# Optimization experiments

Hardware: AMD Instinct MI355X
Metric: run time of the kernel (lower is better)

The kernel has to match this reference:

```python
import jax, jax.numpy as jnp
import numpy as np

EMBED_DIM = 1024
NUM_HEADS = 16
HEAD_DIM = EMBED_DIM // NUM_HEADS
B, T = 4, 2048


def setup_inputs() -> dict:
    key = jax.random.key(0)
    k1, k2, k3, k4, k5 = jax.random.split(key, 5)
    s = 0.02
    return {
        "x": jax.random.normal(k1, (B, T, EMBED_DIM), dtype=jnp.float32),
        "w_qkv": jax.random.normal(k2, (EMBED_DIM, 3 * EMBED_DIM), dtype=jnp.float32) * s,
        "b_qkv": jnp.zeros((3 * EMBED_DIM,), dtype=jnp.float32),
        "w_proj": jax.random.normal(k3, (EMBED_DIM, EMBED_DIM), dtype=jnp.float32) * s,
        "b_proj": jnp.zeros((EMBED_DIM,), dtype=jnp.float32),
    }


def reference(x, w_qkv, b_qkv, w_proj, b_proj):
    Bx, Tx, C = x.shape
    H, D = NUM_HEADS, HEAD_DIM
    qkv = x @ w_qkv + b_qkv                      # [B,T,3C]
    qkv = qkv.reshape(Bx, Tx, 3, H, D)
    q = qkv[:, :, 0].transpose(0, 2, 1, 3)       # [B,H,T,D]
    k = qkv[:, :, 1].transpose(0, 2, 1, 3)
    v = qkv[:, :, 2].transpose(0, 2, 1, 3)
    scale = 1.0 / jnp.sqrt(jnp.asarray(D, dtype=x.dtype))
    att = jnp.einsum("bhqd,bhkd->bhqk", q, k) * scale   # [B,H,T,T]
    causal = jnp.tril(jnp.ones((Tx, Tx), dtype=bool))
    att = jnp.where(causal[None, None], att, jnp.asarray(-jnp.inf, dtype=att.dtype))
    att = jax.nn.softmax(att, axis=-1)
    y = jnp.einsum("bhqk,bhkd->bhqd", att, v)            # [B,H,T,D]
    y = y.transpose(0, 2, 1, 3).reshape(Bx, Tx, C)
    return y @ w_proj + b_proj
```

## Files before the change

### kernel.cpp

```cpp
#include <hip/hip_runtime.h>
#include <hip/hip_bf16.h>

typedef __bf16 bf16_t;
typedef __attribute__((ext_vector_type(4))) __bf16 bf16x4;
typedef __attribute__((ext_vector_type(8))) __bf16 bf16x8;
typedef __attribute__((ext_vector_type(4))) float f32x4;
typedef __attribute__((ext_vector_type(16))) float f32x16;
typedef __attribute__((ext_vector_type(4))) unsigned int uint4v;

__device__ __forceinline__ void async_copy16(const void* g, void* lds) {
  __builtin_amdgcn_global_load_lds(
      (const __attribute__((address_space(1))) unsigned int*)g,
      (__attribute__((address_space(3))) unsigned int*)lds, 16, 0, 0);
}

__device__ __forceinline__ unsigned pkbf(float lo, float hi) {
  unsigned short a = __builtin_bit_cast(unsigned short, (bf16_t)lo);
  unsigned short b = __builtin_bit_cast(unsigned short, (bf16_t)hi);
  return (unsigned)a | ((unsigned)b << 16);
}

__device__ __forceinline__ float swap_add(float v) {
  return v + __shfl_xor(v, 32);
}

__global__ __launch_bounds__(256) void cast_f32_bf16(
    const float* __restrict__ in, bf16_t* __restrict__ out, long n8) {
  long i = (long)blockIdx.x * blockDim.x + threadIdx.x;
  if (i >= n8) return;
  const float4* p = (const float4*)(in + i * 8);
  float4 a = p[0], b = p[1];
  bf16x8 o;
  o[0] = (bf16_t)a.x; o[1] = (bf16_t)a.y; o[2] = (bf16_t)a.z; o[3] = (bf16_t)a.w;
  o[4] = (bf16_t)b.x; o[5] = (bf16_t)b.y; o[6] = (bf16_t)b.z; o[7] = (bf16_t)b.w;
  *(bf16x8*)(out + i * 8) = o;
}

__global__ __launch_bounds__(256) void transpose_cast(
    const float* __restrict__ in, bf16_t* __restrict__ out, int R, int C) {
  __shared__ float tile[32][33];
  int r0 = blockIdx.y * 32, c0 = blockIdx.x * 32;
  int tx = threadIdx.x, ty = threadIdx.y;
#pragma unroll
  for (int j = 0; j < 32; j += 8)
    tile[ty + j][tx] = in[(size_t)(r0 + ty + j) * C + c0 + tx];
  __syncthreads();
#pragma unroll
  for (int j = 0; j < 32; j += 8)
    out[(size_t)(c0 + ty + j) * R + r0 + tx] = (bf16_t)tile[tx][ty + j];
}

template <int MODE>
__global__ __launch_bounds__(256, 2) void gemm_db(
    const bf16_t* __restrict__ A, const bf16_t* __restrict__ Bt,
    const float* __restrict__ bias, int M, int N, int K,
    bf16_t* __restrict__ Qo, bf16_t* __restrict__ Ko, bf16_t* __restrict__ Vo,
    float* __restrict__ Fo) {
  constexpr int BK = 64;
  __shared__ bf16_t As[2][128 * BK];
  __shared__ bf16_t Bs[2][128 * BK];
  const int tid = threadIdx.x;
  const int wid = tid >> 6, lane = tid & 63;
  const int wr = wid >> 1, wc = wid & 1;
  const int g = lane >> 4, c = lane & 15;
  const int nwg = gridDim.x * gridDim.y;
  const int lid = blockIdx.y * gridDim.x + blockIdx.x;
  const int swz = (lid & 7) * (nwg >> 3) + (lid >> 3);
  const int m0 = (swz / gridDim.x) * 128, n0 = (swz % gridDim.x) * 128;
  const int lrow = lane >> 3;
  const int lseg = lane & 7;

  f32x4 acc[4][4] = {};
  const int NT = K >> 6;

#define STAGE(BUF, T)                                                         \
  {                                                                           \
    _Pragma("unroll") for (int cc = 0; cc < 4; ++cc) {                        \
      int chunk = cc * 4 + wid;                                               \
      int row = chunk * 8 + lrow;                                             \
      int seg = lseg ^ (row & 7);                                             \
      async_copy16(A + (size_t)(m0 + row) * K + (T)*BK + seg * 8,             \
                   &As[BUF][chunk * 512]);                                    \
    }                                                                         \
    _Pragma("unroll") for (int cc = 0; cc < 4; ++cc) {                        \
      int chunk = cc * 4 + wid;                                               \
      int row = chunk * 8 + lrow;                                             \
      int seg = lseg ^ (row & 7);                                             \
      async_copy16(Bt + (size_t)(n0 + row) * K + (T)*BK + seg * 8,            \
                   &Bs[BUF][chunk * 512]);                                    \
    }                                                                         \
  }

  STAGE(0, 0);
  __syncthreads();

  for (int t = 0; t < NT; ++t) {
    const int buf = t & 1;
    if (t + 1 < NT) STAGE(buf ^ 1, t + 1);
#pragma unroll
    for (int ks = 0; ks < 2; ++ks) {
      bf16x8 af[4], bfr[4];
#pragma unroll
      for (int m = 0; m < 4; ++m) {
        int row = wr * 64 + m * 16 + c;
        int seg = (ks * 4 + g) ^ (row & 7);
        af[m] = *(const bf16x8*)&As[buf][row * 64 + seg * 8];
      }
#pragma unroll
      for (int n = 0; n < 4; ++n) {
        int row = wc * 64 + n * 16 + c;
        int seg = (ks * 4 + g) ^ (row & 7);
        bfr[n] = *(const bf16x8*)&Bs[buf][row * 64 + seg * 8];
      }
#pragma unroll
      for (int m = 0; m < 4; ++m)
#pragma unroll
        for (int n = 0; n < 4; ++n)
          acc[m][n] =
              __builtin_amdgcn_mfma_f32_16x16x32_bf16(af[m], bfr[n], acc[m][n], 0, 0, 0);
    }
    __syncthreads();
  }
#undef STAGE

  if (MODE == 1) {
#pragma unroll
    for (int m = 0; m < 4; ++m) {
      int grow = m0 + wr * 64 + m * 16 + g * 4;
#pragma unroll
      for (int n = 0; n < 4; ++n) {
        int gcol = n0 + wc * 64 + n * 16 + c;
        float bs = bias[gcol];
#pragma unroll
        for (int i = 0; i < 4; ++i)
          Fo[(size_t)(grow + i) * N + gcol] = acc[m][n][i] + bs;
      }
    }
  } else {
    constexpr float QSC = 0.125f * 1.44269504088896f;
#pragma unroll
    for (int m = 0; m < 4; ++m) {
      int grow = m0 + wr * 64 + m * 16 + g * 4;
#pragma unroll
      for (int n = 0; n < 4; ++n) {
        int gcol = n0 + wc * 64 + n * 16 + c;
        float bs = bias[gcol];
        int sel = gcol >> 10;
        int h = (gcol >> 6) & 15;
        int d = gcol & 63;
        if (sel < 2) {
          bf16_t* dst = (sel == 0) ? Qo : Ko;
          float scl = (sel == 0) ? QSC : 1.0f;
#pragma unroll
          for (int i = 0; i < 4; ++i) {
            int row = grow + i;
            int b = row >> 11, t = row & 2047;
            dst[(((size_t)(b * 16 + h)) * 2048 + t) * 64 + d] =
                (bf16_t)((acc[m][n][i] + bs) * scl);
          }
        } else {
          int b = grow >> 11, t = grow & 2047;
          bf16x4 v;
#pragma unroll
          for (int i = 0; i < 4; ++i) v[i] = (bf16_t)(acc[m][n][i] + bs);
          *(bf16x4*)&Vo[(((size_t)(b * 16 + h)) * 64 + d) * 2048 + t] = v;
        }
      }
    }
  }
}

__global__ __launch_bounds__(256, 4) void attn_fwd(
    const bf16_t* __restrict__ Qg_, const bf16_t* __restrict__ Kg_,
    const bf16_t* __restrict__ Vtg_, bf16_t* __restrict__ Y) {
  __shared__ bf16_t Ks[2][64 * 64];
  __shared__ bf16_t Vs[2][64 * 64];
  const int tid = threadIdx.x, wid = tid >> 6, lane = tid & 63;
  const int l31 = lane & 31, hi = lane >> 5;
  const int bh = blockIdx.x;
  const int b = bh >> 4, h = bh & 15;
  const bf16_t* Qg = Qg_ + (size_t)bh * 2048 * 64;
  const bf16_t* Kg = Kg_ + (size_t)bh * 2048 * 64;
  const bf16_t* Vtg = Vtg_ + (size_t)bh * 64 * 2048;

  const int qt = 15 - blockIdx.y;
  const int q0 = qt * 128;
  const int qw = q0 + wid * 32 + l31;
  const int qmaxw = q0 + wid * 32 + 31;
  const int NT = 2 * qt + 2;

  bf16x8 qf[4];
#pragma unroll
  for (int ks = 0; ks < 4; ++ks)
    qf[ks] = *(const bf16x8*)&Qg[(size_t)qw * 64 + ks * 16 + hi * 8];

  f32x4 sa = {};
  f32x16 ot0 = {}, ot1 = {};

#pragma unroll
  for (int cc = 0; cc < 2; ++cc) {
    int chunk = wid * 2 + cc;
    int row = chunk * 8 + (lane >> 3);
    int seg = (lane & 7) ^ (row & 7);
    async_copy16(Kg + (size_t)row * 64 + seg * 8, &Ks[0][chunk * 512]);
    async_copy16(Vtg + (size_t)row * 2048 + seg * 8, &Vs[0][chunk * 512]);
  }
  __syncthreads();

  for (int kt = 0; kt < NT; ++kt) {
    const int buf = kt & 1;
    if (kt + 1 < NT) {
#pragma unroll
      for (int cc = 0; cc < 2; ++cc) {
        int chunk = wid * 2 + cc;
        int row = chunk * 8 + (lane >> 3);
        int seg = (lane & 7) ^ (row & 7);
        async_copy16(Kg + (size_t)((kt + 1) * 64 + row) * 64 + seg * 8,
                     &Ks[buf ^ 1][chunk * 512]);
        async_copy16(Vtg + (size_t)row * 2048 + (kt + 1) * 64 + seg * 8,
                     &Vs[buf ^ 1][chunk * 512]);
      }
    }
    const int kv0 = kt * 64;
    if (kv0 <= qmaxw) {
      f32x16 st0 = {}, st1 = {};
      __builtin_amdgcn_s_setprio(1);
#pragma unroll
      for (int ks = 0; ks < 4; ++ks) {
        int segb = ks * 2 + hi;
        {
          int row = l31;
          bf16x8 kf = *(const bf16x8*)&Ks[buf][row * 64 + (segb ^ (row & 7)) * 8];
          st0 = __builtin_amdgcn_mfma_f32_32x32x16_bf16(kf, qf[ks], st0, 0, 0, 0);
        }
        {
          int row = 32 + l31;
          bf16x8 kf = *(const bf16x8*)&Ks[buf][row * 64 + (segb ^ (row & 7)) * 8];
          st1 = __builtin_amdgcn_mfma_f32_32x32x16_bf16(kf, qf[ks], st1, 0, 0, 0);
        }
      }
      __builtin_amdgcn_s_setprio(0);
      if (kv0 + 63 > qw) {
#pragma unroll
        for (int r = 0; r < 16; ++r) {
          int kvl = (r & 3) + 8 * (r >> 2) + 4 * hi;
          if (kv0 + kvl > qw) st0[r] = -1e30f;
          if (kv0 + 32 + kvl > qw) st1[r] = -1e30f;
        }
      }
#pragma unroll
      for (int r = 0; r < 16; ++r) {
        st0[r] = exp2f(st0[r]);
        st1[r] = exp2f(st1[r]);
      }
#pragma unroll
      for (int r = 0; r < 4; ++r)
        sa[r] += ((st0[r] + st0[r + 4]) + (st0[r + 8] + st0[r + 12])) +
                 ((st1[r] + st1[r + 4]) + (st1[r + 8] + st1[r + 12]));
      bf16x8 pb[4];
#pragma unroll
      for (int nt = 0; nt < 2; ++nt) {
#pragma unroll
        for (int s = 0; s < 2; ++s) {
          float p0 = nt ? st1[8 * s + 0] : st0[8 * s + 0];
          float p1 = nt ? st1[8 * s + 1] : st0[8 * s + 1];
          float p2 = nt ? st1[8 * s + 2] : st0[8 * s + 2];
          float p3 = nt ? st1[8 * s + 3] : st0[8 * s + 3];
          float p4 = nt ? st1[8 * s + 4] : st0[8 * s + 4];
          float p5 = nt ? st1[8 * s + 5] : st0[8 * s + 5];
          float p6 = nt ? st1[8 * s + 6] : st0[8 * s + 6];
          float p7 = nt ? st1[8 * s + 7] : st0[8 * s + 7];
          unsigned a0 = pkbf(p0, p1), a1 = pkbf(p2, p3);
          unsigned b0 = pkbf(p4, p5), b1 = pkbf(p6, p7);
          unsigned t0 = (unsigned)__shfl_xor((int)(hi ? a0 : b0), 32);
          unsigned t1 = (unsigned)__shfl_xor((int)(hi ? a1 : b1), 32);
          uint4v words;
          words[0] = hi ? t0 : a0;
          words[1] = hi ? t1 : a1;
          words[2] = hi ? b0 : t0;
          words[3] = hi ? b1 : t1;
          pb[nt * 2 + s] = __builtin_bit_cast(bf16x8, words);
        }
      }
      __builtin_amdgcn_s_setprio(1);
#pragma unroll
      for (int ks2 = 0; ks2 < 4; ++ks2) {
        int segb = ks2 * 2 + hi;
        {
          int row = l31;
          bf16x8 vf = *(const bf16x8*)&Vs[buf][row * 64 + (segb ^ (row & 7)) * 8];
          ot0 = __builtin_amdgcn_mfma_f32_32x32x16_bf16(vf, pb[ks2], ot0, 0, 0, 0);
        }
        {
          int row = 32 + l31;
          bf16x8 vf = *(const bf16x8*)&Vs[buf][row * 64 + (segb ^ (row & 7)) * 8];
          ot1 = __builtin_amdgcn_mfma_f32_32x32x16_bf16(vf, pb[ks2], ot1, 0, 0, 0);
        }
      }
      __builtin_amdgcn_s_setprio(0);
    }
    __syncthreads();
  }

  float l = swap_add((sa[0] + sa[1]) + (sa[2] + sa[3]));
  float inv = 1.0f / l;
  size_t yrow = ((size_t)b * 2048 + qw) * 1024 + h * 64;
#pragma unroll
  for (int rq = 0; rq < 4; ++rq) {
    int dbase = 8 * rq + 4 * hi;
    bf16x4 v0, v1;
#pragma unroll
    for (int j = 0; j < 4; ++j) {
      v0[j] = (bf16_t)(ot0[rq * 4 + j] * inv);
      v1[j] = (bf16_t)(ot1[rq * 4 + j] * inv);
    }
    *(bf16x4*)&Y[yrow + dbase] = v0;
    *(bf16x4*)&Y[yrow + 32 + dbase] = v1;
  }
}

extern "C" void kernel_launch(void* const* d_in, const int* in_sizes, int n_in,
                              void* d_out, int out_size, void* d_ws, size_t ws_size,
                              hipStream_t stream) {
  (void)in_sizes; (void)n_in; (void)out_size; (void)ws_size;
  const float* x = (const float*)d_in[0];
  const float* w_qkv = (const float*)d_in[1];
  const float* b_qkv = (const float*)d_in[2];
  const float* w_proj = (const float*)d_in[3];
  const float* b_proj = (const float*)d_in[4];
  float* out = (float*)d_out;

  char* ws = (char*)d_ws;
  size_t off = 0;
  bf16_t* xb = (bf16_t*)(ws + off); off += (size_t)8192 * 1024 * 2;
  bf16_t* wqkvT = (bf16_t*)(ws + off); off += (size_t)3072 * 1024 * 2;
  bf16_t* wprojT = (bf16_t*)(ws + off); off += (size_t)1024 * 1024 * 2;
  bf16_t* Qb = (bf16_t*)(ws + off); off += (size_t)8192 * 1024 * 2;
  bf16_t* Kb = (bf16_t*)(ws + off); off += (size_t)8192 * 1024 * 2;
  bf16_t* Vtb = (bf16_t*)(ws + off); off += (size_t)8192 * 1024 * 2;
  bf16_t* Yb = xb;

  cast_f32_bf16<<<4096, 256, 0, stream>>>(x, xb, (long)8192 * 1024 / 8);
  transpose_cast<<<dim3(96, 32), dim3(32, 8), 0, stream>>>(w_qkv, wqkvT, 1024, 3072);
  transpose_cast<<<dim3(32, 32), dim3(32, 8), 0, stream>>>(w_proj, wprojT, 1024, 1024);
  gemm_db<0><<<dim3(24, 64), 256, 0, stream>>>(xb, wqkvT, b_qkv, 8192, 3072, 1024,
                                               Qb, Kb, Vtb, nullptr);
  attn_fwd<<<dim3(64, 16), 256, 0, stream>>>(Qb, Kb, Vtb, Yb);
  gemm_db<1><<<dim3(8, 64), 256, 0, stream>>>(Yb, wprojT, b_proj, 8192, 1024, 1024,
                                              nullptr, nullptr, nullptr, out);
}
```

Before: 179.8 us.

## Split attention KV loop across two wave groups and pair causal q-tiles per block

Attention blocks grow to 512 threads, with two groups of four waves each handling alternating 64-wide KV tiles for the same 128 query rows. Partial outputs and row sums are merged through shared memory before the output is written. Each block processes a complementary pair of causal query tiles (pair and 15-pair) to balance work across blocks. This is meant to cut the serial KV-loop length and fix causal load imbalance, at the cost of 64KB of LDS, extra reduction traffic and barriers, and possibly lower occupancy.

```diff
diff --git a/kernel.cpp b/kernel.cpp
--- a/kernel.cpp
+++ b/kernel.cpp
@@ -170,152 +170,184 @@
   }
 }
 
-__global__ __launch_bounds__(256, 4) void attn_fwd(
+__global__ __launch_bounds__(512, 4) void attn_fwd(
     const bf16_t* __restrict__ Qg_, const bf16_t* __restrict__ Kg_,
     const bf16_t* __restrict__ Vtg_, bf16_t* __restrict__ Y) {
-  __shared__ bf16_t Ks[2][64 * 64];
-  __shared__ bf16_t Vs[2][64 * 64];
+  __shared__ __align__(16) char smem[65536];
+  bf16_t* Ksp = (bf16_t*)smem;
+  bf16_t* Vsp = (bf16_t*)(smem + 32768);
+  float* scr = (float*)smem;
+
   const int tid = threadIdx.x, wid = tid >> 6, lane = tid & 63;
   const int l31 = lane & 31, hi = lane >> 5;
-  const int bh = blockIdx.x;
+  const int grp = wid >> 2, w4 = wid & 3;
+  const int bh = blockIdx.x, pair = blockIdx.y;
   const int b = bh >> 4, h = bh & 15;
   const bf16_t* Qg = Qg_ + (size_t)bh * 2048 * 64;
   const bf16_t* Kg = Kg_ + (size_t)bh * 2048 * 64;
   const bf16_t* Vtg = Vtg_ + (size_t)bh * 64 * 2048;
 
-  const int qt = 15 - blockIdx.y;
-  const int q0 = qt * 128;
-  const int qw = q0 + wid * 32 + l31;
-  const int qmaxw = q0 + wid * 32 + 31;
-  const int NT = 2 * qt + 2;
-
-  bf16x8 qf[4];
-#pragma unroll
-  for (int ks = 0; ks < 4; ++ks)
-    qf[ks] = *(const bf16x8*)&Qg[(size_t)qw * 64 + ks * 16 + hi * 8];
-
-  f32x4 sa = {};
-  f32x16 ot0 = {}, ot1 = {};
-
-#pragma unroll
-  for (int cc = 0; cc < 2; ++cc) {
-    int chunk = wid * 2 + cc;
-    int row = chunk * 8 + (lane >> 3);
-    int seg = (lane & 7) ^ (row & 7);
-    async_copy16(Kg + (size_t)row * 64 + seg * 8, &Ks[0][chunk * 512]);
-    async_copy16(Vtg + (size_t)row * 2048 + seg * 8, &Vs[0][chunk * 512]);
-  }
-  __syncthreads();
-
-  for (int kt = 0; kt < NT; ++kt) {
-    const int buf = kt & 1;
-    if (kt + 1 < NT) {
+  for (int half = 0; half < 2; ++half) {
+    const int qt = half ? (15 - pair) : pair;
+    const int q0 = qt * 128;
+    const int qw = q0 + w4 * 32 + l31;
+    const int qmaxw = q0 + w4 * 32 + 31;
+    const int NITER = qt + 1;
+
+    bf16x8 qf[4];
+#pragma unroll
+    for (int ks = 0; ks < 4; ++ks)
+      qf[ks] = *(const bf16x8*)&Qg[(size_t)qw * 64 + ks * 16 + hi * 8];
+
+    f32x4 sa = {};
+    f32x16 ot0 = {}, ot1 = {};
+
+    {
+      bf16_t* Kd = Ksp + (grp * 2 + 0) * 4096;
+      bf16_t* Vd = Vsp + (grp * 2 + 0) * 4096;
 #pragma unroll
       for (int cc = 0; cc < 2; ++cc) {
-        int chunk = wid * 2 + cc;
+        int chunk = w4 * 2 + cc;
         int row = chunk * 8 + (lane >> 3);
         int seg = (lane & 7) ^ (row & 7);
-        async_copy16(Kg + (size_t)((kt + 1) * 64 + row) * 64 + seg * 8,
-                     &Ks[buf ^ 1][chunk * 512]);
-        async_copy16(Vtg + (size_t)row * 2048 + (kt + 1) * 64 + seg * 8,
-                     &Vs[buf ^ 1][chunk * 512]);
-      }
-    }
-    const int kv0 = kt * 64;
-    if (kv0 <= qmaxw) {
-      f32x16 st0 = {}, st1 = {};
-      __builtin_amdgcn_s_setprio(1);
-#pragma unroll
-      for (int ks = 0; ks < 4; ++ks) {
-        int segb = ks * 2 + hi;
-        {
-          int row = l31;
-          bf16x8 kf = *(const bf16x8*)&Ks[buf][row * 64 + (segb ^ (row & 7)) * 8];
-          st0 = __builtin_amdgcn_mfma_f32_32x32x16_bf16(kf, qf[ks], st0, 0, 0, 0);
-        }
-        {
-          int row = 32 + l31;
-          bf16x8 kf = *(const bf16x8*)&Ks[buf][row * 64 + (segb ^ (row & 7)) * 8];
-          st1 = __builtin_amdgcn_mfma_f32_32x32x16_bf16(kf, qf[ks], st1, 0, 0, 0);
-        }
-      }
-      __builtin_amdgcn_s_setprio(0);
-      if (kv0 + 63 > qw) {
+        async_copy16(Kg + (size_t)(grp * 64 + row) * 64 + seg * 8, Kd + chunk * 512);
+        async_copy16(Vtg + (size_t)row * 2048 + grp * 64 + seg * 8, Vd + chunk * 512);
+      }
+    }
+    __syncthreads();
+
+    for (int i = 0; i < NITER; ++i) {
+      const int buf = i & 1;
+      const int kt = 2 * i + grp;
+      if (i + 1 < NITER) {
+        const int ktn = 2 * (i + 1) + grp;
+        bf16_t* Kd = Ksp + (grp * 2 + (buf ^ 1)) * 4096;
+        bf16_t* Vd = Vsp + (grp * 2 + (buf ^ 1)) * 4096;
+#pragma unroll
+        for (int cc = 0; cc < 2; ++cc) {
+          int chunk = w4 * 2 + cc;
+          int row = chunk * 8 + (lane >> 3);
+          int seg = (lane & 7) ^ (row & 7);
+          async_copy16(Kg + (size_t)(ktn * 64 + row) * 64 + seg * 8, Kd + chunk * 512);
+          async_copy16(Vtg + (size_t)row * 2048 + ktn * 64 + seg * 8, Vd + chunk * 512);
+        }
+      }
+      const int kv0 = kt * 64;
+      if (kv0 <= qmaxw) {
+        const bf16_t* Kb = Ksp + (grp * 2 + buf) * 4096;
+        const bf16_t* Vb = Vsp + (grp * 2 + buf) * 4096;
+        f32x16 st0 = {}, st1 = {};
+        __builtin_amdgcn_s_setprio(1);
+#pragma unroll
+        for (int ks = 0; ks < 4; ++ks) {
+          int segb = ks * 2 + hi;
+          {
+            int row = l31;
+            bf16x8 kf = *(const bf16x8*)&Kb[row * 64 + (segb ^ (row & 7)) * 8];
+            st0 = __builtin_amdgcn_mfma_f32_32x32x16_bf16(kf, qf[ks], st0, 0, 0, 0);
+          }
+          {
+            int row = 32 + l31;
+            bf16x8 kf = *(const bf16x8*)&Kb[row * 64 + (segb ^ (row & 7)) * 8];
+            st1 = __builtin_amdgcn_mfma_f32_32x32x16_bf16(kf, qf[ks], st1, 0, 0, 0);
+          }
+        }
+        __builtin_amdgcn_s_setprio(0);
+        if (kv0 + 63 > qw) {
+#pragma unroll
+          for (int r = 0; r < 16; ++r) {
+            int kvl = (r & 3) + 8 * (r >> 2) + 4 * hi;
+            if (kv0 + kvl > qw) st0[r] = -1e30f;
+            if (kv0 + 32 + kvl > qw) st1[r] = -1e30f;
+          }
+        }
 #pragma unroll
         for (int r = 0; r < 16; ++r) {
-          int kvl = (r & 3) + 8 * (r >> 2) + 4 * hi;
-          if (kv0 + kvl > qw) st0[r] = -1e30f;
-          if (kv0 + 32 + kvl > qw) st1[r] = -1e30f;
-        }
-      }
-#pragma unroll
-      for (int r = 0; r < 16; ++r) {
-        st0[r] = exp2f(st0[r]);
-        st1[r] = exp2f(st1[r]);
-      }
-#pragma unroll
-      for (int r = 0; r < 4; ++r)
-        sa[r] += ((st0[r] + st0[r + 4]) + (st0[r + 8] + st0[r + 12])) +
-                 ((st1[r] + st1[r + 4]) + (st1[r + 8] + st1[r + 12]));
-      bf16x8 pb[4];
-#pragma unroll
-      for (int nt = 0; nt < 2; ++nt) {
-#pragma unroll
-        for (int s = 0; s < 2; ++s) {
-          float p0 = nt ? st1[8 * s + 0] : st0[8 * s + 0];
-          float p1 = nt ? st1[8 * s + 1] : st0[8 * s + 1];
-          float p2 = nt ? st1[8 * s + 2] : st0[8 * s + 2];
-          float p3 = nt ? st1[8 * s + 3] : st0[8 * s + 3];
-          float p4 = nt ? st1[8 * s + 4] : st0[8 * s + 4];
-          float p5 = nt ? st1[8 * s + 5] : st0[8 * s + 5];
-          float p6 = nt ? st1[8 * s + 6] : st0[8 * s + 6];
-          float p7 = nt ? st1[8 * s + 7] : st0[8 * s + 7];
-          unsigned a0 = pkbf(p0, p1), a1 = pkbf(p2, p3);
-          unsigned b0 = pkbf(p4, p5), b1 = pkbf(p6, p7);
-          unsigned t0 = (unsigned)__shfl_xor((int)(hi ? a0 : b0), 32);
-          unsigned t1 = (unsigned)__shfl_xor((int)(hi ? a1 : b1), 32);
-          uint4v words;
-          words[0] = hi ? t0 : a0;
-          words[1] = hi ? t1 : a1;
-          words[2] = hi ? b0 : t0;
-          words[3] = hi ? b1 : t1;
-          pb[nt * 2 + s] = __builtin_bit_cast(bf16x8, words);
-        }
-      }
-      __builtin_amdgcn_s_setprio(1);
-#pragma unroll
-      for (int ks2 = 0; ks2 < 4; ++ks2) {
-        int segb = ks2 * 2 + hi;
-        {
-          int row = l31;
-          bf16x8 vf = *(const bf16x8*)&Vs[buf][row * 64 + (segb ^ (row & 7)) * 8];
-          ot0 = __builtin_amdgcn_mfma_f32_32x32x16_bf16(vf, pb[ks2], ot0, 0, 0, 0);
-        }
-        {
-          int row = 32 + l31;
-          bf16x8 vf = *(const bf16x8*)&Vs[buf][row * 64 + (segb ^ (row & 7)) * 8];
-          ot1 = __builtin_amdgcn_mfma_f32_32x32x16_bf16(vf, pb[ks2], ot1, 0, 0, 0);
-        }
-      }
-      __builtin_amdgcn_s_setprio(0);
+          st0[r] = exp2f(st0[r]);
+          st1[r] = exp2f(st1[r]);
+        }
+#pragma unroll
+        for (int r = 0; r < 4; ++r)
+          sa[r] += ((st0[r] + st0[r + 4]) + (st0[r + 8] + st0[r + 12])) +
+                   ((st1[r] + st1[r + 4]) + (st1[r + 8] + st1[r + 12]));
+        bf16x8 pb[4];
+#pragma unroll
+        for (int nt = 0; nt < 2; ++nt) {
+#pragma unroll
+          for (int s = 0; s < 2; ++s) {
+            float p0 = nt ? st1[8 * s + 0] : st0[8 * s + 0];
+            float p1 = nt ? st1[8 * s + 1] : st0[8 * s + 1];
+            float p2 = nt ? st1[8 * s + 2] : st0[8 * s + 2];
+            float p3 = nt ? st1[8 * s + 3] : st0[8 * s + 3];
+            float p4 = nt ? st1[8 * s + 4] : st0[8 * s + 4];
+            float p5 = nt ? st1[8 * s + 5] : st0[8 * s + 5];
+            float p6 = nt ? st1[8 * s + 6] : st0[8 * s + 6];
+            float p7 = nt ? st1[8 * s + 7] : st0[8 * s + 7];
+            unsigned a0 = pkbf(p0, p1), a1 = pkbf(p2, p3);
+            unsigned b0 = pkbf(p4, p5), b1 = pkbf(p6, p7);
+            unsigned t0 = (unsigned)__shfl_xor((int)(hi ? a0 : b0), 32);
+            unsigned t1 = (unsigned)__shfl_xor((int)(hi ? a1 : b1), 32);
+            uint4v words;
+            words[0] = hi ? t0 : a0;
+            words[1] = hi ? t1 : a1;
+            words[2] = hi ? b0 : t0;
+            words[3] = hi ? b1 : t1;
+            pb[nt * 2 + s] = __builtin_bit_cast(bf16x8, words);
+          }
+        }
+        __builtin_amdgcn_s_setprio(1);
+#pragma unroll
+        for (int ks2 = 0; ks2 < 4; ++ks2) {
+          int segb = ks2 * 2 + hi;
+          {
+            int row = l31;
+            bf16x8 vf = *(const bf16x8*)&Vb[row * 64 + (segb ^ (row & 7)) * 8];
+            ot0 = __builtin_amdgcn_mfma_f32_32x32x16_bf16(vf, pb[ks2], ot0, 0, 0, 0);
+          }
+          {
+            int row = 32 + l31;
+            bf16x8 vf = *(const bf16x8*)&Vb[row * 64 + (segb ^ (row & 7)) * 8];
+            ot1 = __builtin_amdgcn_mfma_f32_32x32x16_bf16(vf, pb[ks2], ot1, 0, 0, 0);
+          }
+        }
+        __builtin_amdgcn_s_setprio(0);
+      }
+      __syncthreads();
+    }
+
+    if (grp == 1) {
+#pragma unroll
+      for (int r = 0; r < 16; ++r) scr[(w4 * 36 + r) * 64 + lane] = ot0[r];
+#pragma unroll
+      for (int r = 0; r < 16; ++r) scr[(w4 * 36 + 16 + r) * 64 + lane] = ot1[r];
+#pragma unroll
+      for (int r = 0; r < 4; ++r) scr[(w4 * 36 + 32 + r) * 64 + lane] = sa[r];
     }
     __syncthreads();
-  }
-
-  float l = swap_add((sa[0] + sa[1]) + (sa[2] + sa[3]));
-  float inv = 1.0f / l;
-  size_t yrow = ((size_t)b * 2048 + qw) * 1024 + h * 64;
-#pragma unroll
-  for (int rq = 0; rq < 4; ++rq) {
-    int dbase = 8 * rq + 4 * hi;
-    bf16x4 v0, v1;
-#pragma unroll
-    for (int j = 0; j < 4; ++j) {
-      v0[j] = (bf16_t)(ot0[rq * 4 + j] * inv);
-      v1[j] = (bf16_t)(ot1[rq * 4 + j] * inv);
-    }
-    *(bf16x4*)&Y[yrow + dbase] = v0;
-    *(bf16x4*)&Y[yrow + 32 + dbase] = v1;
+    if (grp == 0) {
+#pragma unroll
+      for (int r = 0; r < 16; ++r) ot0[r] += scr[(w4 * 36 + r) * 64 + lane];
+#pragma unroll
+      for (int r = 0; r < 16; ++r) ot1[r] += scr[(w4 * 36 + 16 + r) * 64 + lane];
+#pragma unroll
+      for (int r = 0; r < 4; ++r) sa[r] += scr[(w4 * 36 + 32 + r) * 64 + lane];
+      float l = swap_add((sa[0] + sa[1]) + (sa[2] + sa[3]));
+      float inv = 1.0f / l;
+      size_t yrow = ((size_t)b * 2048 + qw) * 1024 + h * 64;
+#pragma unroll
+      for (int rq = 0; rq < 4; ++rq) {
+        int dbase = 8 * rq + 4 * hi;
+        bf16x4 v0, v1;
+#pragma unroll
+        for (int j = 0; j < 4; ++j) {
+          v0[j] = (bf16_t)(ot0[rq * 4 + j] * inv);
+          v1[j] = (bf16_t)(ot1[rq * 4 + j] * inv);
+        }
+        *(bf16x4*)&Y[yrow + dbase] = v0;
+        *(bf16x4*)&Y[yrow + 32 + dbase] = v1;
+      }
+    }
+    __syncthreads();
   }
 }
 
@@ -345,7 +377,7 @@
   transpose_cast<<<dim3(32, 32), dim3(32, 8), 0, stream>>>(w_proj, wprojT, 1024, 1024);
   gemm_db<0><<<dim3(24, 64), 256, 0, stream>>>(xb, wqkvT, b_qkv, 8192, 3072, 1024,
                                                Qb, Kb, Vtb, nullptr);
-  attn_fwd<<<dim3(64, 16), 256, 0, stream>>>(Qb, Kb, Vtb, Yb);
+  attn_fwd<<<dim3(64, 8), 512, 0, stream>>>(Qb, Kb, Vtb, Yb);
   gemm_db<1><<<dim3(8, 64), 256, 0, stream>>>(Yb, wprojT, b_proj, 8192, 1024, 1024,
                                               nullptr, nullptr, nullptr, out);
 }
```

Result: no change. 181.2 us (+0.8%).

## Store K/V in MFMA fragment order and load directly from global, dropping LDS

Applied to the files above, without the earlier changes.

The QKV GEMM epilogue now writes K and V in a pre-swizzled per-tile fragment layout, so each lane's MFMA operand is one contiguous 16-byte global load. The attention kernel drops the LDS double buffer, async copies and block barriers, and reads K/V fragments straight from global memory (L2/cache), breaking out early past the causal limit. This removes LDS traffic and synchronisation, but each of the four waves now loads the same K/V tile from global without explicit prefetch, so it leans on cache bandwidth and latency hiding through occupancy. The V epilogue stores become scattered 8-byte writes.

```diff
diff --git a/kernel.cpp b/kernel.cpp
--- a/kernel.cpp
+++ b/kernel.cpp
@@ -148,22 +148,33 @@
         int sel = gcol >> 10;
         int h = (gcol >> 6) & 15;
         int d = gcol & 63;
-        if (sel < 2) {
-          bf16_t* dst = (sel == 0) ? Qo : Ko;
-          float scl = (sel == 0) ? QSC : 1.0f;
+        if (sel == 0) {
 #pragma unroll
           for (int i = 0; i < 4; ++i) {
             int row = grow + i;
             int b = row >> 11, t = row & 2047;
-            dst[(((size_t)(b * 16 + h)) * 2048 + t) * 64 + d] =
-                (bf16_t)((acc[m][n][i] + bs) * scl);
+            Qo[(((size_t)(b * 16 + h)) * 2048 + t) * 64 + d] =
+                (bf16_t)((acc[m][n][i] + bs) * QSC);
+          }
+        } else if (sel == 1) {
+          int ks = d >> 4, hid = (d >> 3) & 1, jd = d & 7;
+#pragma unroll
+          for (int i = 0; i < 4; ++i) {
+            int row = grow + i;
+            int b = row >> 11, t = row & 2047;
+            int kt = t >> 6, half = (t >> 5) & 1, tl = t & 31;
+            Ko[(((size_t)(b * 16 + h) * 32 + kt) * 8 + ks * 2 + half) * 512 +
+               (hid * 32 + tl) * 8 + jd] = (bf16_t)(acc[m][n][i] + bs);
           }
         } else {
           int b = grow >> 11, t = grow & 2047;
+          int kt = t >> 6, ks2 = (t & 63) >> 4, hiv = (t >> 3) & 1, j0 = t & 7;
+          int dhalf = d >> 5, dl = d & 31;
           bf16x4 v;
 #pragma unroll
           for (int i = 0; i < 4; ++i) v[i] = (bf16_t)(acc[m][n][i] + bs);
-          *(bf16x4*)&Vo[(((size_t)(b * 16 + h)) * 64 + d) * 2048 + t] = v;
+          *(bf16x4*)&Vo[(((size_t)(b * 16 + h) * 32 + kt) * 8 + ks2 * 2 + dhalf) * 512 +
+                        (hiv * 32 + dl) * 8 + j0] = v;
         }
       }
     }
@@ -171,17 +182,15 @@
 }
 
 __global__ __launch_bounds__(256, 4) void attn_fwd(
-    const bf16_t* __restrict__ Qg_, const bf16_t* __restrict__ Kg_,
-    const bf16_t* __restrict__ Vtg_, bf16_t* __restrict__ Y) {
-  __shared__ bf16_t Ks[2][64 * 64];
-  __shared__ bf16_t Vs[2][64 * 64];
+    const bf16_t* __restrict__ Qg_, const bf16_t* __restrict__ Kf_,
+    const bf16_t* __restrict__ Vf_, bf16_t* __restrict__ Y) {
   const int tid = threadIdx.x, wid = tid >> 6, lane = tid & 63;
   const int l31 = lane & 31, hi = lane >> 5;
   const int bh = blockIdx.x;
   const int b = bh >> 4, h = bh & 15;
   const bf16_t* Qg = Qg_ + (size_t)bh * 2048 * 64;
-  const bf16_t* Kg = Kg_ + (size_t)bh * 2048 * 64;
-  const bf16_t* Vtg = Vtg_ + (size_t)bh * 64 * 2048;
+  const bf16_t* Kf = Kf_ + (size_t)bh * 32 * 4096;
+  const bf16_t* Vf = Vf_ + (size_t)bh * 32 * 4096;
 
   const int qt = 15 - blockIdx.y;
   const int q0 = qt * 128;
@@ -197,109 +206,72 @@
   f32x4 sa = {};
   f32x16 ot0 = {}, ot1 = {};
 
-#pragma unroll
-  for (int cc = 0; cc < 2; ++cc) {
-    int chunk = wid * 2 + cc;
-    int row = chunk * 8 + (lane >> 3);
-    int seg = (lane & 7) ^ (row & 7);
-    async_copy16(Kg + (size_t)row * 64 + seg * 8, &Ks[0][chunk * 512]);
-    async_copy16(Vtg + (size_t)row * 2048 + seg * 8, &Vs[0][chunk * 512]);
-  }
-  __syncthreads();
-
   for (int kt = 0; kt < NT; ++kt) {
-    const int buf = kt & 1;
-    if (kt + 1 < NT) {
-#pragma unroll
-      for (int cc = 0; cc < 2; ++cc) {
-        int chunk = wid * 2 + cc;
-        int row = chunk * 8 + (lane >> 3);
-        int seg = (lane & 7) ^ (row & 7);
-        async_copy16(Kg + (size_t)((kt + 1) * 64 + row) * 64 + seg * 8,
-                     &Ks[buf ^ 1][chunk * 512]);
-        async_copy16(Vtg + (size_t)row * 2048 + (kt + 1) * 64 + seg * 8,
-                     &Vs[buf ^ 1][chunk * 512]);
-      }
-    }
     const int kv0 = kt * 64;
-    if (kv0 <= qmaxw) {
-      f32x16 st0 = {}, st1 = {};
-      __builtin_amdgcn_s_setprio(1);
-#pragma unroll
-      for (int ks = 0; ks < 4; ++ks) {
-        int segb = ks * 2 + hi;
-        {
-          int row = l31;
-          bf16x8 kf = *(const bf16x8*)&Ks[buf][row * 64 + (segb ^ (row & 7)) * 8];
-          st0 = __builtin_amdgcn_mfma_f32_32x32x16_bf16(kf, qf[ks], st0, 0, 0, 0);
-        }
-        {
-          int row = 32 + l31;
-          bf16x8 kf = *(const bf16x8*)&Ks[buf][row * 64 + (segb ^ (row & 7)) * 8];
-          st1 = __builtin_amdgcn_mfma_f32_32x32x16_bf16(kf, qf[ks], st1, 0, 0, 0);
-        }
-      }
-      __builtin_amdgcn_s_setprio(0);
-      if (kv0 + 63 > qw) {
-#pragma unroll
-        for (int r = 0; r < 16; ++r) {
-          int kvl = (r & 3) + 8 * (r >> 2) + 4 * hi;
-          if (kv0 + kvl > qw) st0[r] = -1e30f;
-          if (kv0 + 32 + kvl > qw) st1[r] = -1e30f;
-        }
-      }
+    if (kv0 > qmaxw) break;
+    const bf16_t* Kt = Kf + kt * 4096;
+    const bf16_t* Vt = Vf + kt * 4096;
+    f32x16 st0 = {}, st1 = {};
+    __builtin_amdgcn_s_setprio(1);
+#pragma unroll
+    for (int ks = 0; ks < 4; ++ks) {
+      bf16x8 kf0 = *(const bf16x8*)&Kt[(ks * 2 + 0) * 512 + lane * 8];
+      bf16x8 kf1 = *(const bf16x8*)&Kt[(ks * 2 + 1) * 512 + lane * 8];
+      st0 = __builtin_amdgcn_mfma_f32_32x32x16_bf16(kf0, qf[ks], st0, 0, 0, 0);
+      st1 = __builtin_amdgcn_mfma_f32_32x32x16_bf16(kf1, qf[ks], st1, 0, 0, 0);
+    }
+    __builtin_amdgcn_s_setprio(0);
+    if (kv0 + 63 > qw) {
 #pragma unroll
       for (int r = 0; r < 16; ++r) {
-        st0[r] = exp2f(st0[r]);
-        st1[r] = exp2f(st1[r]);
-      }
-#pragma unroll
-      for (int r = 0; r < 4; ++r)
-        sa[r] += ((st0[r] + st0[r + 4]) + (st0[r + 8] + st0[r + 12])) +
-                 ((st1[r] + st1[r + 4]) + (st1[r + 8] + st1[r + 12]));
-      bf16x8 pb[4];
-#pragma unroll
-      for (int nt = 0; nt < 2; ++nt) {
-#pragma unroll
-        for (int s = 0; s < 2; ++s) {
-          float p0 = nt ? st1[8 * s + 0] : st0[8 * s + 0];
-          float p1 = nt ? st1[8 * s + 1] : st0[8 * s + 1];
-          float p2 = nt ? st1[8 * s + 2] : st0[8 * s + 2];
-          float p3 = nt ? st1[8 * s + 3] : st0[8 * s + 3];
-          float p4 = nt ? st1[8 * s + 4] : st0[8 * s + 4];
-          float p5 = nt ? st1[8 * s + 5] : st0[8 * s + 5];
-          float p6 = nt ? st1[8 * s + 6] : st0[8 * s + 6];
-          float p7 = nt ? st1[8 * s + 7] : st0[8 * s + 7];
-          unsigned a0 = pkbf(p0, p1), a1 = pkbf(p2, p3);
-          unsigned b0 = pkbf(p4, p5), b1 = pkbf(p6, p7);
-          unsigned t0 = (unsigned)__shfl_xor((int)(hi ? a0 : b0), 32);
-          unsigned t1 = (unsigned)__shfl_xor((int)(hi ? a1 : b1), 32);
-          uint4v words;
-          words[0] = hi ? t0 : a0;
-          words[1] = hi ? t1 : a1;
-          words[2] = hi ? b0 : t0;
-          words[3] = hi ? b1 : t1;
-          pb[nt * 2 + s] = __builtin_bit_cast(bf16x8, words);
-        }
-      }
-      __builtin_amdgcn_s_setprio(1);
-#pragma unroll
-      for (int ks2 = 0; ks2 < 4; ++ks2) {
-        int segb = ks2 * 2 + hi;
-        {
-          int row = l31;
-          bf16x8 vf = *(const bf16x8*)&Vs[buf][row * 64 + (segb ^ (row & 7)) * 8];
-          ot0 = __builtin_amdgcn_mfma_f32_32x32x16_bf16(vf, pb[ks2], ot0, 0, 0, 0);
-        }
-        {
-          int row = 32 + l31;
-          bf16x8 vf = *(const bf16x8*)&Vs[buf][row * 64 + (segb ^ (row & 7)) * 8];
-          ot1 = __builtin_amdgcn_mfma_f32_32x32x16_bf16(vf, pb[ks2], ot1, 0, 0, 0);
-        }
-      }
-      __builtin_amdgcn_s_setprio(0);
-    }
-    __syncthreads();
+        int kvl = (r & 3) + 8 * (r >> 2) + 4 * hi;
+        if (kv0 + kvl > qw) st0[r] = -1e30f;
+        if (kv0 + 32 + kvl > qw) st1[r] = -1e30f;
+      }
+    }
+#pragma unroll
+    for (int r = 0; r < 16; ++r) {
+      st0[r] = exp2f(st0[r]);
+      st1[r] = exp2f(st1[r]);
+    }
+#pragma unroll
+    for (int r = 0; r < 4; ++r)
+      sa[r] += ((st0[r] + st0[r + 4]) + (st0[r + 8] + st0[r + 12])) +
+               ((st1[r] + st1[r + 4]) + (st1[r + 8] + st1[r + 12]));
+    bf16x8 pb[4];
+#pragma unroll
+    for (int nt = 0; nt < 2; ++nt) {
+#pragma unroll
+      for (int s = 0; s < 2; ++s) {
+        float p0 = nt ? st1[8 * s + 0] : st0[8 * s + 0];
+        float p1 = nt ? st1[8 * s + 1] : st0[8 * s + 1];
+        float p2 = nt ? st1[8 * s + 2] : st0[8 * s + 2];
+        float p3 = nt ? st1[8 * s + 3] : st0[8 * s + 3];
+        float p4 = nt ? st1[8 * s + 4] : st0[8 * s + 4];
+        float p5 = nt ? st1[8 * s + 5] : st0[8 * s + 5];
+        float p6 = nt ? st1[8 * s + 6] : st0[8 * s + 6];
+        float p7 = nt ? st1[8 * s + 7] : st0[8 * s + 7];
+        unsigned a0 = pkbf(p0, p1), a1 = pkbf(p2, p3);
+        unsigned b0 = pkbf(p4, p5), b1 = pkbf(p6, p7);
+        unsigned t0 = (unsigned)__shfl_xor((int)(hi ? a0 : b0), 32);
+        unsigned t1 = (unsigned)__shfl_xor((int)(hi ? a1 : b1), 32);
+        uint4v words;
+        words[0] = hi ? t0 : a0;
+        words[1] = hi ? t1 : a1;
+        words[2] = hi ? b0 : t0;
+        words[3] = hi ? b1 : t1;
+        pb[nt * 2 + s] = __builtin_bit_cast(bf16x8, words);
+      }
+    }
+    __builtin_amdgcn_s_setprio(1);
+#pragma unroll
+    for (int ks2 = 0; ks2 < 4; ++ks2) {
+      bf16x8 vf0 = *(const bf16x8*)&Vt[(ks2 * 2 + 0) * 512 + lane * 8];
+      bf16x8 vf1 = *(const bf16x8*)&Vt[(ks2 * 2 + 1) * 512 + lane * 8];
+      ot0 = __builtin_amdgcn_mfma_f32_32x32x16_bf16(vf0, pb[ks2], ot0, 0, 0, 0);
+      ot1 = __builtin_amdgcn_mfma_f32_32x32x16_bf16(vf1, pb[ks2], ot1, 0, 0, 0);
+    }
+    __builtin_amdgcn_s_setprio(0);
   }
 
   float l = swap_add((sa[0] + sa[1]) + (sa[2] + sa[3]));
@@ -336,16 +308,16 @@
   bf16_t* wqkvT = (bf16_t*)(ws + off); off += (size_t)3072 * 1024 * 2;
   bf16_t* wprojT = (bf16_t*)(ws + off); off += (size_t)1024 * 1024 * 2;
   bf16_t* Qb = (bf16_t*)(ws + off); off += (size_t)8192 * 1024 * 2;
-  bf16_t* Kb = (bf16_t*)(ws + off); off += (size_t)8192 * 1024 * 2;
-  bf16_t* Vtb = (bf16_t*)(ws + off); off += (size_t)8192 * 1024 * 2;
+  bf16_t* Kfb = (bf16_t*)(ws + off); off += (size_t)8192 * 1024 * 2;
+  bf16_t* Vfb = (bf16_t*)(ws + off); off += (size_t)8192 * 1024 * 2;
   bf16_t* Yb = xb;
 
   cast_f32_bf16<<<4096, 256, 0, stream>>>(x, xb, (long)8192 * 1024 / 8);
   transpose_cast<<<dim3(96, 32), dim3(32, 8), 0, stream>>>(w_qkv, wqkvT, 1024, 3072);
   transpose_cast<<<dim3(32, 32), dim3(32, 8), 0, stream>>>(w_proj, wprojT, 1024, 1024);
   gemm_db<0><<<dim3(24, 64), 256, 0, stream>>>(xb, wqkvT, b_qkv, 8192, 3072, 1024,
-                                               Qb, Kb, Vtb, nullptr);
-  attn_fwd<<<dim3(64, 16), 256, 0, stream>>>(Qb, Kb, Vtb, Yb);
+                                               Qb, Kfb, Vfb, nullptr);
+  attn_fwd<<<dim3(64, 16), 256, 0, stream>>>(Qb, Kfb, Vfb, Yb);
   gemm_db<1><<<dim3(8, 64), 256, 0, stream>>>(Yb, wprojT, b_proj, 8192, 1024, 1024,
                                               nullptr, nullptr, nullptr, out);
 }
```

Measured after the change: 193.5 us. 1.08x slower.

## Use 256x256-tile 8-wave GEMM with split-K-half pipelining for QKV projection

Applied to the files above, without the earlier changes.

Replaces the 128x128 QKV projection GEMM with a 512-thread kernel using 256x256 output tiles, each wave computing 128x64. Each 64-wide K step is split into two 32-wide halves, so the next half's async LDS load overlaps the current half's MFMAs. Also adds an XOR-swizzled LDS layout and raises wave priority around the MFMA blocks. Larger tiles double operand reuse per LDS load and cut global traffic. The cost is more registers (128 accumulator floats per thread) and only 384 workgroups on the GPU, which risks lower occupancy and a wave-quantization tail.

```diff
diff --git a/kernel.cpp b/kernel.cpp
--- a/kernel.cpp
+++ b/kernel.cpp
@@ -50,11 +50,146 @@
     out[(size_t)(c0 + ty + j) * R + r0 + tx] = (bf16_t)tile[tx][ty + j];
 }
 
-template <int MODE>
+__global__ __launch_bounds__(512, 2) void gemm_8p(
+    const bf16_t* __restrict__ A, const bf16_t* __restrict__ Bt,
+    const float* __restrict__ bias, int M, int N, int K,
+    bf16_t* __restrict__ Qo, bf16_t* __restrict__ Ko, bf16_t* __restrict__ Vo) {
+  __shared__ bf16_t As[2][2][256 * 32];
+  __shared__ bf16_t Bs[2][2][256 * 32];
+  const int tid = threadIdx.x;
+  const int wid = tid >> 6, lane = tid & 63;
+  const int wm = wid >> 2, wn = wid & 3;
+  const int g = lane >> 4, c = lane & 15;
+  const int nwg = gridDim.x * gridDim.y;
+  const int lid = blockIdx.y * gridDim.x + blockIdx.x;
+  const int swz = (lid & 7) * (nwg >> 3) + (lid >> 3);
+  const int m0 = (swz / gridDim.x) * 256, n0 = (swz % gridDim.x) * 256;
+  const int srow_in_chunk = lane >> 2;
+  const int sseg = lane & 3;
+
+  f32x4 acc[8][4] = {};
+  const int NT = K >> 6;
+
+#define STAGE_KH(BUF, T, KH)                                                  \
+  {                                                                           \
+    _Pragma("unroll") for (int cc = 0; cc < 2; ++cc) {                        \
+      int chunk = cc * 8 + wid;                      \
+      int row = chunk * 16 + srow_in_chunk;                                   \
+      int segl = sseg ^ ((row >> 1) & 3);        \
+      async_copy16(A + (size_t)(m0 + row) * K + (T)*64 + (KH)*32 + segl * 8,  \
+                   &As[BUF][KH][chunk * 512]);                                \
+    }                                                                         \
+    _Pragma("unroll") for (int cc = 0; cc < 2; ++cc) {                        \
+      int chunk = cc * 8 + wid;                                               \
+      int row = chunk * 16 + srow_in_chunk;                                   \
+      int segl = sseg ^ ((row >> 1) & 3);                                     \
+      async_copy16(Bt + (size_t)(n0 + row) * K + (T)*64 + (KH)*32 + segl * 8, \
+                   &Bs[BUF][KH][chunk * 512]);                                \
+    }                                                                         \
+  }
+
+  STAGE_KH(0, 0, 0);
+  STAGE_KH(0, 0, 1);
+  asm volatile("s_waitcnt vmcnt(4)" ::: "memory");
+  __builtin_amdgcn_s_barrier();
+
+  for (int t = 0; t < NT; ++t) {
+    const int buf = t & 1, nbuf = buf ^ 1;
+    if (t + 1 < NT) STAGE_KH(nbuf, t + 1, 0);
+    {
+      bf16x8 af[8], bfr[4];
+#pragma unroll
+      for (int mr = 0; mr < 8; ++mr) {
+        int row = wm * 128 + mr * 16 + c;
+        int segp = g ^ ((row >> 1) & 3);
+        af[mr] = *(const bf16x8*)&As[buf][0][row * 32 + segp * 8];
+      }
+#pragma unroll
+      for (int n = 0; n < 4; ++n) {
+        int row = wn * 64 + n * 16 + c;
+        int segp = g ^ ((row >> 1) & 3);
+        bfr[n] = *(const bf16x8*)&Bs[buf][0][row * 32 + segp * 8];
+      }
+      __builtin_amdgcn_s_setprio(1);
+#pragma unroll
+      for (int mr = 0; mr < 8; ++mr)
+#pragma unroll
+        for (int n = 0; n < 4; ++n)
+          acc[mr][n] =
+              __builtin_amdgcn_mfma_f32_16x16x32_bf16(af[mr], bfr[n], acc[mr][n], 0, 0, 0);
+      __builtin_amdgcn_s_setprio(0);
+    }
+    if (t == NT - 1)
+      asm volatile("s_waitcnt vmcnt(0)" ::: "memory");
+    else
+      asm volatile("s_waitcnt vmcnt(4)" ::: "memory");
+    __builtin_amdgcn_s_barrier();
+    if (t + 1 < NT) STAGE_KH(nbuf, t + 1, 1);
+    {
+      bf16x8 af[8], bfr[4];
+#pragma unroll
+      for (int mr = 0; mr < 8; ++mr) {
+        int row = wm * 128 + mr * 16 + c;
+        int segp = g ^ ((row >> 1) & 3);
+        af[mr] = *(const bf16x8*)&As[buf][1][row * 32 + segp * 8];
+      }
+#pragma unroll
+      for (int n = 0; n < 4; ++n) {
+        int row = wn * 64 + n * 16 + c;
+        int segp = g ^ ((row >> 1) & 3);
+        bfr[n] = *(const bf16x8*)&Bs[buf][1][row * 32 + segp * 8];
+      }
+      __builtin_amdgcn_s_setprio(1);
+#pragma unroll
+      for (int mr = 0; mr < 8; ++mr)
+#pragma unroll
+        for (int n = 0; n < 4; ++n)
+          acc[mr][n] =
+              __builtin_amdgcn_mfma_f32_16x16x32_bf16(af[mr], bfr[n], acc[mr][n], 0, 0, 0);
+      __builtin_amdgcn_s_setprio(0);
+    }
+    if (t < NT - 1) {
+      asm volatile("s_waitcnt vmcnt(4)" ::: "memory");
+      __builtin_amdgcn_s_barrier();
+    }
+  }
+#undef STAGE_KH
+
+  constexpr float QSC = 0.125f * 1.44269504088896f;
+#pragma unroll
+  for (int mr = 0; mr < 8; ++mr) {
+    int grow = m0 + wm * 128 + mr * 16 + g * 4;
+#pragma unroll
+    for (int n = 0; n < 4; ++n) {
+      int gcol = n0 + wn * 64 + n * 16 + c;
+      float bs = bias[gcol];
+      int sel = gcol >> 10;
+      int h = (gcol >> 6) & 15;
+      int d = gcol & 63;
+      if (sel < 2) {
+        bf16_t* dst = (sel == 0) ? Qo : Ko;
+        float scl = (sel == 0) ? QSC : 1.0f;
+#pragma unroll
+        for (int i = 0; i < 4; ++i) {
+          int row = grow + i;
+          int b = row >> 11, tt = row & 2047;
+          dst[(((size_t)(b * 16 + h)) * 2048 + tt) * 64 + d] =
+              (bf16_t)((acc[mr][n][i] + bs) * scl);
+        }
+      } else {
+        int b = grow >> 11, tt = grow & 2047;
+        bf16x4 v;
+#pragma unroll
+        for (int i = 0; i < 4; ++i) v[i] = (bf16_t)(acc[mr][n][i] + bs);
+        *(bf16x4*)&Vo[(((size_t)(b * 16 + h)) * 64 + d) * 2048 + tt] = v;
+      }
+    }
+  }
+}
+
 __global__ __launch_bounds__(256, 2) void gemm_db(
     const bf16_t* __restrict__ A, const bf16_t* __restrict__ Bt,
     const float* __restrict__ bias, int M, int N, int K,
-    bf16_t* __restrict__ Qo, bf16_t* __restrict__ Ko, bf16_t* __restrict__ Vo,
     float* __restrict__ Fo) {
   constexpr int BK = 64;
   __shared__ bf16_t As[2][128 * BK];
@@ -123,49 +258,16 @@
   }
 #undef STAGE
 
-  if (MODE == 1) {
-#pragma unroll
-    for (int m = 0; m < 4; ++m) {
-      int grow = m0 + wr * 64 + m * 16 + g * 4;
-#pragma unroll
-      for (int n = 0; n < 4; ++n) {
-        int gcol = n0 + wc * 64 + n * 16 + c;
-        float bs = bias[gcol];
-#pragma unroll
-        for (int i = 0; i < 4; ++i)
-          Fo[(size_t)(grow + i) * N + gcol] = acc[m][n][i] + bs;
-      }
-    }
-  } else {
-    constexpr float QSC = 0.125f * 1.44269504088896f;
-#pragma unroll
-    for (int m = 0; m < 4; ++m) {
-      int grow = m0 + wr * 64 + m * 16 + g * 4;
-#pragma unroll
-      for (int n = 0; n < 4; ++n) {
-        int gcol = n0 + wc * 64 + n * 16 + c;
-        float bs = bias[gcol];
-        int sel = gcol >> 10;
-        int h = (gcol >> 6) & 15;
-        int d = gcol & 63;
-        if (sel < 2) {
-          bf16_t* dst = (sel == 0) ? Qo : Ko;
-          float scl = (sel == 0) ? QSC : 1.0f;
-#pragma unroll
-          for (int i = 0; i < 4; ++i) {
-            int row = grow + i;
-            int b = row >> 11, t = row & 2047;
-            dst[(((size_t)(b * 16 + h)) * 2048 + t) * 64 + d] =
-                (bf16_t)((acc[m][n][i] + bs) * scl);
-          }
-        } else {
-          int b = grow >> 11, t = grow & 2047;
-          bf16x4 v;
-#pragma unroll
-          for (int i = 0; i < 4; ++i) v[i] = (bf16_t)(acc[m][n][i] + bs);
-          *(bf16x4*)&Vo[(((size_t)(b * 16 + h)) * 64 + d) * 2048 + t] = v;
-        }
-      }
+#pragma unroll
+  for (int m = 0; m < 4; ++m) {
+    int grow = m0 + wr * 64 + m * 16 + g * 4;
+#pragma unroll
+    for (int n = 0; n < 4; ++n) {
+      int gcol = n0 + wc * 64 + n * 16 + c;
+      float bs = bias[gcol];
+#pragma unroll
+      for (int i = 0; i < 4; ++i)
+        Fo[(size_t)(grow + i) * N + gcol] = acc[m][n][i] + bs;
     }
   }
 }
@@ -343,9 +445,8 @@
   cast_f32_bf16<<<4096, 256, 0, stream>>>(x, xb, (long)8192 * 1024 / 8);
   transpose_cast<<<dim3(96, 32), dim3(32, 8), 0, stream>>>(w_qkv, wqkvT, 1024, 3072);
   transpose_cast<<<dim3(32, 32), dim3(32, 8), 0, stream>>>(w_proj, wprojT, 1024, 1024);
-  gemm_db<0><<<dim3(24, 64), 256, 0, stream>>>(xb, wqkvT, b_qkv, 8192, 3072, 1024,
-                                               Qb, Kb, Vtb, nullptr);
+  gemm_8p<<<dim3(12, 32), 512, 0, stream>>>(xb, wqkvT, b_qkv, 8192, 3072, 1024,
+                                            Qb, Kb, Vtb);
   attn_fwd<<<dim3(64, 16), 256, 0, stream>>>(Qb, Kb, Vtb, Yb);
-  gemm_db<1><<<dim3(8, 64), 256, 0, stream>>>(Yb, wprojT, b_proj, 8192, 1024, 1024,
-                                              nullptr, nullptr, nullptr, out);
-}
+  gemm_db<<<dim3(8, 64), 256, 0, stream>>>(Yb, wprojT, b_proj, 8192, 1024, 1024, out);
+}
```

Measured after the change: 198.2 us. 10.2% more time.
